# Kernel optimization log

Measured on AMD Instinct MI355X. Metric: run time of the kernel, lower is better.

Reference implementation:

```python
import jax, jax.numpy as jnp
import numpy as np

L, S, R, NUM_RESNET = 6, 2, 3, 3
N = 2 ** L            # 64 blocks per axis
NX = N * S            # 128 grid points per axis
NCART_SIDE = 80
NCART = NCART_SIDE ** 2


def _perm_idx(L_, l):
    delta = 2 ** (L_ - l - 1)
    t = np.tile(np.arange(2) * delta, delta) + np.repeat(np.arange(delta), 2)
    t = np.tile(t, 2 ** l) + np.repeat(np.arange(2 ** l) * 2 ** (L_ - l), 2 ** (L_ - l))
    return jnp.asarray(t)


def _switch_idx(L_):
    h = L_ // 2
    t = np.tile(np.arange(2 ** h) * 2 ** h, 2 ** h) + np.repeat(np.arange(2 ** h), 2 ** h)
    return jnp.asarray(t)


def _bmm2(x, g_left, g_right):
    # x: (B,p,i,q,j). Right block-diag GEMM on (q,j), then left block-diag GEMM on (p,i).
    y = jnp.einsum('bpiqj,qjk->bpiqk', x, g_right)
    return jnp.einsum('bpiqk,pio->bpoqk', y, g_left)


def _complex_layer(xr, xi, p):
    # p: stacked (r1,i1,r2,i2,r3,i3,r4,i4); complex-style cross products of the original.
    r1, i1, r2, i2, r3, i3, r4, i4 = p
    yr = _bmm2(xr, r1, r1) + _bmm2(xr, i1, i1) + _bmm2(xi, r2, i2) + _bmm2(xi, i2, r2)
    yi = _bmm2(xi, r3, r3) + _bmm2(xi, i3, i3) + _bmm2(xr, r4, i4) + _bmm2(xr, i4, r4)
    return yr, yi


def _u_layer(xr, xi, p):
    ur1, ui1, ur2, ui2, ur3, ui3, ur4, ui4 = p
    return (_bmm2(xr, ur1, ur1) + _bmm2(xr, ui2, ui2)
            + _bmm2(xi, ur3, ui3) + _bmm2(xi, ui4, ur4))


def _permute(yr, yi, idx):
    yr = jnp.take(jnp.take(yr, idx, axis=1), idx, axis=3)
    yi = jnp.take(jnp.take(yi, idx, axis=1), idx, axis=3)
    return yr, yi


def _merge(y):  # (B,N,R,N,R) -> (B,N/2,2R,N/2,2R)
    return y.reshape(y.shape[0], N // 2, 2 * R, N // 2, 2 * R)


def _split(y):  # inverse of _merge
    return y.reshape(y.shape[0], N, R, N, R)


def reference(x, Vp, Hp, Mp, Gp, Up, cart_mat, r_index):
    B = x.shape[0]
    xr = x[..., 0].reshape(B, N, S, N, S)
    xi = x[..., 1].reshape(B, N, S, N, S)
    yr, yi = _complex_layer(xr, xi, Vp)                       # (B,N,R,N,R)
    for li, l in enumerate(range(L - 1, L // 2 - 1, -1)):     # H stages (permute then merge-GEMM)
        yr, yi = _permute(yr, yi, _perm_idx(L, l))
        yr, yi = _complex_layer(_merge(yr), _merge(yi), Hp[li])
        yr, yi = _split(yr), _split(yi)
    yr, yi = _permute(yr, yi, _switch_idx(L))                 # middle switch shuffle
    for k in range(NUM_RESNET):                               # residual M blocks
        zr, zi = _complex_layer(yr, yi, Mp[k])
        yr, yi = yr + zr, yi + zi
    for li, l in enumerate(range(L // 2 - 1, -1, -1)):        # G stages (merge-GEMM then permute)
        yr, yi = _complex_layer(_merge(yr), _merge(yi), Gp[li])
        yr, yi = _split(yr), _split(yi)
        yr, yi = _permute(yr, yi, _perm_idx(L, l))
    y = _u_layer(yr, yi, Up).reshape(B, NX * NX)              # real output, (B,NX,NX) flattened
    y = jnp.take(y, r_index, axis=1)                          # polar reindexing
    out = y @ cart_mat.T                                      # polar -> cartesian interpolation
    return out.reshape(B, NCART_SIDE, NCART_SIDE)


def setup_inputs() -> dict:
    key = jax.random.key(0)
    ks = jax.random.split(key, 9)
    B = 128
    x = jax.random.normal(ks[0], (B, NX, NX, 2), dtype=jnp.float32)
    Vp = jax.random.normal(ks[1], (8, N, S, R), dtype=jnp.float32) * 0.35
    Hp = jax.random.normal(ks[2], (L // 2, 8, N // 2, 2 * R, 2 * R), dtype=jnp.float32) * 0.2
    Mp = jax.random.normal(ks[3], (NUM_RESNET, 8, N, R, R), dtype=jnp.float32) * 0.25
    Gp = jax.random.normal(ks[4], (L // 2, 8, N // 2, 2 * R, 2 * R), dtype=jnp.float32) * 0.2
    Up = jax.random.normal(ks[5], (8, N, R, S), dtype=jnp.float32) * 0.35
    cart_mat = jax.random.normal(ks[6], (NCART, NX * NX), dtype=jnp.float32) * 0.01
    r_index = jax.random.permutation(ks[7], NX * NX).astype(jnp.int32)
    return {"x": x, "Vp": Vp, "Hp": Hp, "Mp": Mp, "Gp": Gp, "Up": Up,
            "cart_mat": cart_mat, "r_index": r_index}
```

## Files before the change

kernel.cpp:

```cpp
#include <hip/hip_runtime.h>


typedef _Float16 f16;
typedef __attribute__((ext_vector_type(8))) short sx8;
typedef __attribute__((ext_vector_type(4))) float fx4;
typedef __attribute__((ext_vector_type(8))) unsigned short usx8;
typedef __attribute__((ext_vector_type(4))) unsigned short usx4;

__device__ __forceinline__ unsigned short f2bf(float f) {
  unsigned u = __builtin_bit_cast(unsigned, f);
  u = (u + 0x7FFFu + ((u >> 16) & 1u)) >> 16;
  return (unsigned short)u;
}
__device__ __forceinline__ float bf2f(unsigned short h) {
  return __builtin_bit_cast(float, ((unsigned)h) << 16);
}

template<int ID>
__device__ __forceinline__ int rp_apply(int k) {
  if constexpr (ID == 0) { return k; }
  else if constexpr (ID == 3) { return (k & 7) * 8 + (k >> 3); }
  else {
    constexpr int l = (ID == 1) ? 4 : (ID == 2) ? 3 : (ID == 4) ? 2 : (ID == 5) ? 1 : 0;
    constexpr int d = 1 << (5 - l);
    constexpr int m2 = 2 * d;
    int g = k / m2, r = k % m2;
    return g * m2 + (r & 1) * d + (r >> 1);
  }
}

__device__ __forceinline__ void term_decode(int t, int& lm, int& rm,
                                            bool& useXi, bool& toYi) {
  lm = (t < 2) ? t : (t < 4) ? (t + 4) : (t - 2);
  rm = (t >= 2 && t <= 5) ? (lm ^ 1) : lm;
  useXi = (t >= 4);
  toYi = (t >> 1) & 1;
}

#define SMEM_BYTES 36864

__device__ __forceinline__ void layer6(int g, int b, int P, int Q,
                                       const float* __restrict__ wp,
                                       const f16* ldsX, float* Y0, float* Y1,
                                       f16* __restrict__ yr,
                                       f16* __restrict__ yi) {
  int lm0, rm0, lm1, rm1;
  switch (g) {
    case 0:  lm0 = 0; rm0 = 0; lm1 = 1; rm1 = 1; break;
    case 1:  lm0 = 6; rm0 = 7; lm1 = 7; rm1 = 6; break;
    case 2:  lm0 = 2; rm0 = 3; lm1 = 3; rm1 = 2; break;
    default: lm0 = 4; rm0 = 4; lm1 = 5; rm1 = 5; break;
  }
  const int xbase = (g & 2) ? 36 : 0;
  float X[36], Y[36];
#pragma unroll
  for (int k = 0; k < 36; ++k) X[k] = (float)ldsX[(xbase + k) * 128 + b];
#pragma unroll
  for (int k = 0; k < 36; ++k) Y[k] = 0.f;

  for (int tt = 0; tt < 2; ++tt) {
    const int lm = tt ? lm1 : lm0;
    const int rm = tt ? rm1 : rm0;
    const float* Lw = wp + ((size_t)lm * 32 + P) * 36;
    const float* Rw = wp + ((size_t)rm * 32 + Q) * 36;
#pragma unroll
    for (int i = 0; i < 6; ++i) {
      float tk[6] = {0.f, 0.f, 0.f, 0.f, 0.f, 0.f};
#pragma unroll
      for (int j = 0; j < 6; ++j) {
        float xv = X[i * 6 + j];
#pragma unroll
        for (int k = 0; k < 6; ++k) tk[k] += xv * Rw[j * 6 + k];
      }
#pragma unroll
      for (int o = 0; o < 6; ++o) {
        float lv = Lw[i * 6 + o];
#pragma unroll
        for (int k = 0; k < 6; ++k) Y[o * 6 + k] += lv * tk[k];
      }
    }
  }
  __syncthreads();
  if (g == 2) {
#pragma unroll
    for (int k = 0; k < 36; ++k) Y0[k * 128 + b] = Y[k];
  } else if (g == 3) {
#pragma unroll
    for (int k = 0; k < 36; ++k) Y1[k * 128 + b] = Y[k];
  }
  __syncthreads();
  if (g == 0) {
#pragma unroll
    for (int k = 0; k < 36; ++k) {
      float v = Y[k] + Y0[k * 128 + b];
      yr[((size_t)((P * 6 + k / 6) * 192 + Q * 6 + k % 6)) * 128 + b] = (f16)v;
    }
  } else if (g == 1) {
#pragma unroll
    for (int k = 0; k < 36; ++k) {
      float v = Y[k] + Y1[k * 128 + b];
      yi[((size_t)((P * 6 + k / 6) * 192 + Q * 6 + k % 6)) * 128 + b] = (f16)v;
    }
  }
}

__global__ __launch_bounds__(256) void k_transpose(const float* __restrict__ x,
                                                   f16* __restrict__ xtr,
                                                   f16* __restrict__ xti) {
  __shared__ float ls[2][32][129];
  const int t = threadIdx.x;
  const int u = blockIdx.x;
  const int v0 = blockIdx.y * 32;
  for (int it = 0; it < 32; ++it) {
    int b = it * 4 + (t >> 6);
    int r = t & 63;
    int v = r >> 1, ch = r & 1;
    ls[ch][v][b] = x[(((size_t)b * 128 + u) * 128 + (v0 + v)) * 2 + ch];
  }
  __syncthreads();
  for (int it = 0; it < 32; ++it) {
    int idx = it * 256 + t;
    int ch = idx >> 12;
    int v = (idx >> 7) & 31;
    int b = idx & 127;
    f16* dst = ch ? xti : xtr;
    dst[((size_t)(u * 128 + v0 + v)) * 128 + b] = (f16)ls[ch][v][b];
  }
}

__global__ __launch_bounds__(512, 4) void k_vh(const f16* __restrict__ xtr,
                                               const f16* __restrict__ xti,
                                               f16* __restrict__ yr,
                                               f16* __restrict__ yi,
                                               const float* __restrict__ vp,
                                               const float* __restrict__ hp) {
  __shared__ __align__(16) char smem[SMEM_BYTES];
  f16* ldsX = (f16*)smem;
  float* Y0 = (float*)smem;
  float* Y1 = (float*)(smem + 18432);
  const int t = threadIdx.x;
  const int P = blockIdx.x, Q = blockIdx.y;
  const int g = __builtin_amdgcn_readfirstlane(t >> 7);
  const int b = t & 127;

  const int pp = g >> 1, qq = g & 1;
  const int p = 2 * P + pp, q = 2 * Q + qq;
  float Xr[4], Xi[4];
#pragma unroll
  for (int i = 0; i < 2; ++i)
#pragma unroll
    for (int j = 0; j < 2; ++j) {
      size_t off = ((size_t)((4 * P + 2 * pp + i) * 128 + (4 * Q + 2 * qq + j))) * 128 + b;
      Xr[i * 2 + j] = (float)xtr[off];
      Xi[i * 2 + j] = (float)xti[off];
    }
  float Ar[9], Ai[9];
#pragma unroll
  for (int k = 0; k < 9; ++k) { Ar[k] = 0.f; Ai[k] = 0.f; }
  for (int tt = 0; tt < 8; ++tt) {
    int lm, rm; bool useXi, toYi;
    term_decode(tt, lm, rm, useXi, toYi);
    const float* Lw = vp + ((size_t)lm * 64 + p) * 6;
    const float* Rw = vp + ((size_t)rm * 64 + q) * 6;
#pragma unroll
    for (int i = 0; i < 2; ++i) {
      float x0, x1;
      if (useXi) { x0 = Xi[i * 2 + 0]; x1 = Xi[i * 2 + 1]; }
      else       { x0 = Xr[i * 2 + 0]; x1 = Xr[i * 2 + 1]; }
      float t0 = x0 * Rw[0] + x1 * Rw[3];
      float t1 = x0 * Rw[1] + x1 * Rw[4];
      float t2 = x0 * Rw[2] + x1 * Rw[5];
      if (toYi) {
#pragma unroll
        for (int o = 0; o < 3; ++o) {
          float lv = Lw[i * 3 + o];
          Ai[o*3+0] += lv * t0; Ai[o*3+1] += lv * t1; Ai[o*3+2] += lv * t2;
        }
      } else {
#pragma unroll
        for (int o = 0; o < 3; ++o) {
          float lv = Lw[i * 3 + o];
          Ar[o*3+0] += lv * t0; Ar[o*3+1] += lv * t1; Ar[o*3+2] += lv * t2;
        }
      }
    }
  }
#pragma unroll
  for (int o = 0; o < 3; ++o)
#pragma unroll
    for (int k = 0; k < 3; ++k) {
      int ch = (3 * pp + o) * 6 + (3 * qq + k);
      ldsX[ch * 128 + b] = (f16)Ar[o * 3 + k];
      ldsX[(36 + ch) * 128 + b] = (f16)Ai[o * 3 + k];
    }
  __syncthreads();
  layer6(g, b, P, Q, hp, ldsX, Y0, Y1, yr, yi);
}

template<int PERM>
__global__ __launch_bounds__(512, 4) void k_hg(const f16* __restrict__ xr,
                                               const f16* __restrict__ xi,
                                               f16* __restrict__ yr,
                                               f16* __restrict__ yi,
                                               const float* __restrict__ wp) {
  __shared__ __align__(16) char smem[SMEM_BYTES];
  f16* ldsX = (f16*)smem;
  float* Y0 = (float*)smem;
  float* Y1 = (float*)(smem + 18432);
  const int t = threadIdx.x;
  const int P = blockIdx.x, Q = blockIdx.y;

  for (int r = 0; r < 3; ++r) {
    int idx = t + r * 512;
    if (idx < 1152) {
      int c = idx >> 4, o8 = (idx & 15) * 8;
      int cc = (c < 36) ? c : c - 36;
      int I = cc / 6, J = cc % 6;
      int grow = rp_apply<PERM>(2 * P + I / 3) * 3 + I % 3;
      int gcol = rp_apply<PERM>(2 * Q + J / 3) * 3 + J % 3;
      const f16* src = (c < 36) ? xr : xi;
      usx8 v = *(const usx8*)(src + ((size_t)(grow * 192 + gcol)) * 128 + o8);
      *(usx8*)(ldsX + c * 128 + o8) = v;
    }
  }
  __syncthreads();
  const int g = __builtin_amdgcn_readfirstlane(t >> 7);
  const int b = t & 127;
  layer6(g, b, P, Q, wp, ldsX, Y0, Y1, yr, yi);
}

__global__ __launch_bounds__(512, 4) void k_mg(const f16* __restrict__ xr,
                                               const f16* __restrict__ xi,
                                               f16* __restrict__ yr,
                                               f16* __restrict__ yi,
                                               const float* __restrict__ mp,
                                               const float* __restrict__ gp) {
  __shared__ __align__(16) char smem[SMEM_BYTES];
  f16* ldsX = (f16*)smem;
  float* Y0 = (float*)smem;
  float* Y1 = (float*)(smem + 18432);
  const int t = threadIdx.x;
  const int P = blockIdx.x, Q = blockIdx.y;
  const int g = __builtin_amdgcn_readfirstlane(t >> 7);
  const int b = t & 127;

  const int aa = g >> 1, bb = g & 1;
  const int p = 2 * P + aa, q = 2 * Q + bb;
  const int prow = rp_apply<3>(p) * 3, pcol = rp_apply<3>(q) * 3;
  float Xr[9], Xi[9];
#pragma unroll
  for (int i = 0; i < 3; ++i)
#pragma unroll
    for (int j = 0; j < 3; ++j) {
      size_t off = ((size_t)((prow + i) * 192 + (pcol + j))) * 128 + b;
      Xr[i * 3 + j] = (float)xr[off];
      Xi[i * 3 + j] = (float)xi[off];
    }
  for (int lk = 0; lk < 3; ++lk) {
    const float* wp = mp + (size_t)lk * (8 * 64 * 9);
    float Yr9[9], Yi9[9];
#pragma unroll
    for (int k = 0; k < 9; ++k) { Yr9[k] = Xr[k]; Yi9[k] = Xi[k]; }
    for (int tt = 0; tt < 8; ++tt) {
      int lm, rm; bool useXi, toYi;
      term_decode(tt, lm, rm, useXi, toYi);
      const float* Lw = wp + ((size_t)lm * 64 + p) * 9;
      const float* Rw = wp + ((size_t)rm * 64 + q) * 9;
#pragma unroll
      for (int i = 0; i < 3; ++i) {
        float x0, x1, x2;
        if (useXi) { x0 = Xi[i*3+0]; x1 = Xi[i*3+1]; x2 = Xi[i*3+2]; }
        else       { x0 = Xr[i*3+0]; x1 = Xr[i*3+1]; x2 = Xr[i*3+2]; }
        float t0 = x0 * Rw[0] + x1 * Rw[3] + x2 * Rw[6];
        float t1 = x0 * Rw[1] + x1 * Rw[4] + x2 * Rw[7];
        float t2 = x0 * Rw[2] + x1 * Rw[5] + x2 * Rw[8];
        if (toYi) {
#pragma unroll
          for (int o = 0; o < 3; ++o) {
            float lv = Lw[i * 3 + o];
            Yi9[o*3+0] += lv * t0; Yi9[o*3+1] += lv * t1; Yi9[o*3+2] += lv * t2;
          }
        } else {
#pragma unroll
          for (int o = 0; o < 3; ++o) {
            float lv = Lw[i * 3 + o];
            Yr9[o*3+0] += lv * t0; Yr9[o*3+1] += lv * t1; Yr9[o*3+2] += lv * t2;
          }
        }
      }
    }
#pragma unroll
    for (int k = 0; k < 9; ++k) { Xr[k] = Yr9[k]; Xi[k] = Yi9[k]; }
  }
#pragma unroll
  for (int i = 0; i < 3; ++i)
#pragma unroll
    for (int j = 0; j < 3; ++j) {
      int ch = (3 * aa + i) * 6 + (3 * bb + j);
      ldsX[ch * 128 + b] = (f16)Xr[i * 3 + j];
      ldsX[(36 + ch) * 128 + b] = (f16)Xi[i * 3 + j];
    }
  __syncthreads();
  layer6(g, b, P, Q, gp, ldsX, Y0, Y1, yr, yi);
}

__global__ __launch_bounds__(128, 2) void k_u(const f16* __restrict__ xr,
                                              const f16* __restrict__ xi,
                                              unsigned short* __restrict__ ut,
                                              const float* __restrict__ wp) {
  const int b = threadIdx.x;
  const int p = blockIdx.x, q = blockIdx.y;
  int rrow[3], rcol[3];
#pragma unroll
  for (int i = 0; i < 3; ++i) {
    rrow[i] = rp_apply<6>(p) * 3 + i;
    rcol[i] = rp_apply<6>(q) * 3 + i;
  }
  float X[9], Y[4] = {0.f, 0.f, 0.f, 0.f};
  auto loadX = [&](const f16* src) {
#pragma unroll
    for (int i = 0; i < 3; ++i)
#pragma unroll
      for (int j = 0; j < 3; ++j)
        X[i * 3 + j] = (float)src[((size_t)(rrow[i] * 192 + rcol[j])) * 128 + b];
  };
  auto term = [&](int lm, int rm) {
    const float* Lw = wp + ((size_t)lm * 64 + p) * 6;
    const float* Rw = wp + ((size_t)rm * 64 + q) * 6;
#pragma unroll
    for (int i = 0; i < 3; ++i) {
      float t0 = X[i*3+0] * Rw[0] + X[i*3+1] * Rw[2] + X[i*3+2] * Rw[4];
      float t1 = X[i*3+0] * Rw[1] + X[i*3+1] * Rw[3] + X[i*3+2] * Rw[5];
      Y[0] += Lw[i*2+0] * t0; Y[1] += Lw[i*2+0] * t1;
      Y[2] += Lw[i*2+1] * t0; Y[3] += Lw[i*2+1] * t1;
    }
  };
  loadX(xr); term(0, 0); term(3, 3);
  loadX(xi); term(4, 5); term(7, 6);
#pragma unroll
  for (int o = 0; o < 2; ++o)
#pragma unroll
    for (int k = 0; k < 2; ++k)
      ut[((size_t)((p * 2 + o) * 128 + (q * 2 + k))) * 128 + b] = f2bf(Y[o * 2 + k]);
}

__global__ __launch_bounds__(256) void k_gather(const unsigned short* __restrict__ ut,
                                                const int* __restrict__ r_index,
                                                unsigned short* __restrict__ yg) {
  __shared__ unsigned short ls[64][130];
  __shared__ int ridx[64];
  const int t = threadIdx.x;
  const int m0 = blockIdx.x * 64;
  if (t < 64) ridx[t] = r_index[m0 + t];
  __syncthreads();
  for (int it = 0; it < 32; ++it) {
    int idx = it * 256 + t;
    int ml = idx >> 7, b = idx & 127;
    ls[ml][b] = ut[(size_t)ridx[ml] * 128 + b];
  }
  __syncthreads();
  int b = t >> 1, half = t & 1;
#pragma unroll
  for (int c = 0; c < 4; ++c) {
    usx8 v;
#pragma unroll
    for (int e = 0; e < 8; ++e) v[e] = ls[half * 32 + c * 8 + e][b];
    *(usx8*)(yg + (size_t)b * 16384 + m0 + half * 32 + c * 8) = v;
  }
}

#define G3_KC 8
#define G3_STEPS 32
#define G3_PITCH 72

__global__ __launch_bounds__(256) void k_gemm3(const unsigned short* __restrict__ yg,
                                               const float* __restrict__ cart,
                                               unsigned short* __restrict__ partial) {
  __shared__ unsigned short Bs[2][64][G3_PITCH];
  const int t = threadIdx.x;
  const int lane = t & 63, w = t >> 6;
  const int kc = blockIdx.x;
  const int c0 = blockIdx.y * 64;
  const int k0 = kc * 2048;

  fx4 acc[2][4];
#pragma unroll
  for (int i = 0; i < 2; ++i)
#pragma unroll
    for (int j = 0; j < 4; ++j) acc[i][j] = (fx4)0.f;

  const unsigned short* aBase = yg + (size_t)(w * 32 + (lane & 15)) * 16384
                                   + k0 + (lane >> 4) * 8;

  auto ldB = [&](int rep, int kpos, fx4* f0, fx4* f1) {
    int c = t + rep * 256;
    const float* p = cart + (size_t)(c0 + (c >> 3)) * 16384 + kpos + (c & 7) * 8;
    *f0 = *(const fx4*)p;
    *f1 = *(const fx4*)(p + 4);
  };
  auto stB = [&](int buf, int rep, fx4 f0, fx4 f1) {
    int c = t + rep * 256;
    usx8 v;
    v[0]=f2bf(f0[0]); v[1]=f2bf(f0[1]); v[2]=f2bf(f0[2]); v[3]=f2bf(f0[3]);
    v[4]=f2bf(f1[0]); v[5]=f2bf(f1[1]); v[6]=f2bf(f1[2]); v[7]=f2bf(f1[3]);
    *(usx8*)(&Bs[buf][c >> 3][(c & 7) * 8]) = v;
  };

  {
    fx4 b00, b01, b10, b11;
    ldB(0, k0, &b00, &b01); ldB(1, k0, &b10, &b11);
    stB(0, 0, b00, b01); stB(0, 1, b10, b11);
  }
  __syncthreads();

  for (int s = 0; s < G3_STEPS; ++s) {
    const int cur = s & 1;
    fx4 b00, b01, b10, b11;
    const bool pf = (s + 1 < G3_STEPS);
    if (pf) {
      int kpos = k0 + (s + 1) * 64;
      ldB(0, kpos, &b00, &b01); ldB(1, kpos, &b10, &b11);
    }
    sx8 af[2][2], bf[4][2];
#pragma unroll
    for (int mi = 0; mi < 2; ++mi)
#pragma unroll
      for (int kk = 0; kk < 2; ++kk)
        af[mi][kk] = *(const sx8*)(aBase + (size_t)mi * 16 * 16384 + s * 64 + kk * 32);
#pragma unroll
    for (int ni = 0; ni < 4; ++ni)
#pragma unroll
      for (int kk = 0; kk < 2; ++kk)
        bf[ni][kk] = *(const sx8*)(&Bs[cur][ni * 16 + (lane & 15)][kk * 32 + (lane >> 4) * 8]);
#pragma unroll
    for (int kk = 0; kk < 2; ++kk)
#pragma unroll
      for (int mi = 0; mi < 2; ++mi)
#pragma unroll
        for (int ni = 0; ni < 4; ++ni)
          acc[mi][ni] = __builtin_amdgcn_mfma_f32_16x16x32_bf16(af[mi][kk], bf[ni][kk], acc[mi][ni], 0, 0, 0);
    if (pf) {
      stB(cur ^ 1, 0, b00, b01); stB(cur ^ 1, 1, b10, b11);
    }
    __syncthreads();
  }

#pragma unroll
  for (int mi = 0; mi < 2; ++mi) {
    int brow = w * 32 + mi * 16 + (lane >> 4) * 4;
#pragma unroll
    for (int ni = 0; ni < 4; ++ni) {
      int cc = c0 + ni * 16 + (lane & 15);
#pragma unroll
      for (int r = 0; r < 4; ++r)
        partial[((size_t)kc * 128 + brow + r) * 6400 + cc] = f2bf(acc[mi][ni][r]);
    }
  }
}

__global__ __launch_bounds__(256) void k_reduce2(const unsigned short* __restrict__ partial,
                                                 float* __restrict__ out) {
  int i = blockIdx.x * 256 + threadIdx.x;
  fx4 s = (fx4)0.f;
#pragma unroll
  for (int kc = 0; kc < G3_KC; ++kc) {
    usx4 v = *(const usx4*)(partial + (size_t)kc * 819200 + (size_t)i * 4);
    s[0] += bf2f(v[0]); s[1] += bf2f(v[1]); s[2] += bf2f(v[2]); s[3] += bf2f(v[3]);
  }
  *(fx4*)(out + (size_t)i * 4) = s;
}

extern "C" void kernel_launch(void* const* d_in, const int* in_sizes, int n_in,
                              void* d_out, int out_size, void* d_ws, size_t ws_size,
                              hipStream_t stream) {
  const float* x    = (const float*)d_in[0];
  const float* Vp   = (const float*)d_in[1];
  const float* Hp   = (const float*)d_in[2];
  const float* Mp   = (const float*)d_in[3];
  const float* Gp   = (const float*)d_in[4];
  const float* Up   = (const float*)d_in[5];
  const float* cart = (const float*)d_in[6];
  const int*   ridx = (const int*)d_in[7];
  float* out = (float*)d_out;
  unsigned short* hb = (unsigned short*)d_ws;

  const size_t PSZ = 4718592;
  f16* P0r = (f16*)(hb);
  f16* P0i = (f16*)(hb + PSZ);
  f16* P1r = (f16*)(hb + 2 * PSZ);
  f16* P1i = (f16*)(hb + 3 * PSZ);
  f16* xtr = (f16*)(hb + 4 * PSZ);
  f16* xti = (f16*)(hb + 4 * PSZ + 2097152);
  unsigned short* ut = hb + 4 * PSZ;
  unsigned short* yg = hb + 4 * PSZ + 2097152;
  unsigned short* partial = hb;

  const size_t HSZ = 8 * 32 * 36;

  k_transpose<<<dim3(128, 4), 256, 0, stream>>>(x, xtr, xti);
  k_vh<<<dim3(32, 32), 512, 0, stream>>>(xtr, xti, P0r, P0i, Vp, Hp + 0 * HSZ);
  k_hg<1><<<dim3(32, 32), 512, 0, stream>>>(P0r, P0i, P1r, P1i, Hp + 1 * HSZ);
  k_hg<2><<<dim3(32, 32), 512, 0, stream>>>(P1r, P1i, P0r, P0i, Hp + 2 * HSZ);
  k_mg<<<dim3(32, 32), 512, 0, stream>>>(P0r, P0i, P1r, P1i, Mp, Gp + 0 * HSZ);
  k_hg<4><<<dim3(32, 32), 512, 0, stream>>>(P1r, P1i, P0r, P0i, Gp + 1 * HSZ);
  k_hg<5><<<dim3(32, 32), 512, 0, stream>>>(P0r, P0i, P1r, P1i, Gp + 2 * HSZ);
  k_u<<<dim3(64, 64), 128, 0, stream>>>(P1r, P1i, ut, Up);
  k_gather<<<dim3(256), 256, 0, stream>>>(ut, ridx, yg);
  k_gemm3<<<dim3(G3_KC, 100), 256, 0, stream>>>(yg, cart, partial);
  k_reduce2<<<dim3(800), 256, 0, stream>>>(partial, out);
  (void)in_sizes; (void)n_in; (void)out_size; (void)ws_size;
}
```

Measured before the change: 308.6 us.

## Stage A tiles through LDS and deepen cartesian GEMM prefetch pipeline

The final polar-to-cartesian GEMM now loads A (the gathered activations) into shared memory cooperatively instead of having each wave read fragments straight from global memory. It also halves the K step to 32 and adds a register-staged, two-step-ahead prefetch, with a triple-buffered B and a double-buffered A. The goal is to hide global-load latency and make A reads coalesced. In exchange it does twice as many iterations and barriers, uses more shared memory, and keeps more registers live for the prefetch.

```diff
diff --git a/kernel.cpp b/kernel.cpp
--- a/kernel.cpp
+++ b/kernel.cpp
@@ -369,14 +369,15 @@
   }
 }
 
-#define G3_KC 8
-#define G3_STEPS 32
-#define G3_PITCH 72
-
-__global__ __launch_bounds__(256) void k_gemm3(const unsigned short* __restrict__ yg,
+#define G4_KC 8
+#define G4_STEPS 64
+#define G4_P 40
+
+__global__ __launch_bounds__(256) void k_gemm4(const unsigned short* __restrict__ yg,
                                                const float* __restrict__ cart,
                                                unsigned short* __restrict__ partial) {
-  __shared__ unsigned short Bs[2][64][G3_PITCH];
+  __shared__ unsigned short As[2][128][G4_P];
+  __shared__ unsigned short Bs[3][64][G4_P];
   const int t = threadIdx.x;
   const int lane = t & 63, w = t >> 6;
   const int kc = blockIdx.x;
@@ -389,59 +390,56 @@
 #pragma unroll
     for (int j = 0; j < 4; ++j) acc[i][j] = (fx4)0.f;
 
-  const unsigned short* aBase = yg + (size_t)(w * 32 + (lane & 15)) * 16384
-                                   + k0 + (lane >> 4) * 8;
-
-  auto ldB = [&](int rep, int kpos, fx4* f0, fx4* f1) {
-    int c = t + rep * 256;
-    const float* p = cart + (size_t)(c0 + (c >> 3)) * 16384 + kpos + (c & 7) * 8;
+  auto ldA = [&](int kpos, usx8* a0, usx8* a1) {
+    int c0i = t, c1i = t + 256;
+    *a0 = *(const usx8*)(yg + (size_t)(c0i >> 2) * 16384 + kpos + (c0i & 3) * 8);
+    *a1 = *(const usx8*)(yg + (size_t)(c1i >> 2) * 16384 + kpos + (c1i & 3) * 8);
+  };
+  auto stA = [&](int buf, usx8 a0, usx8 a1) {
+    int c0i = t, c1i = t + 256;
+    *(usx8*)(&As[buf][c0i >> 2][(c0i & 3) * 8]) = a0;
+    *(usx8*)(&As[buf][c1i >> 2][(c1i & 3) * 8]) = a1;
+  };
+  auto ldB = [&](int kpos, fx4* f0, fx4* f1) {
+    const float* p = cart + (size_t)(c0 + (t >> 2)) * 16384 + kpos + (t & 3) * 8;
     *f0 = *(const fx4*)p;
     *f1 = *(const fx4*)(p + 4);
   };
-  auto stB = [&](int buf, int rep, fx4 f0, fx4 f1) {
-    int c = t + rep * 256;
+  auto stB = [&](int buf, fx4 f0, fx4 f1) {
     usx8 v;
     v[0]=f2bf(f0[0]); v[1]=f2bf(f0[1]); v[2]=f2bf(f0[2]); v[3]=f2bf(f0[3]);
     v[4]=f2bf(f1[0]); v[5]=f2bf(f1[1]); v[6]=f2bf(f1[2]); v[7]=f2bf(f1[3]);
-    *(usx8*)(&Bs[buf][c >> 3][(c & 7) * 8]) = v;
+    *(usx8*)(&Bs[buf][t >> 2][(t & 3) * 8]) = v;
   };
 
+  usx8 rA0, rA1; fx4 rB0, rB1;
   {
-    fx4 b00, b01, b10, b11;
-    ldB(0, k0, &b00, &b01); ldB(1, k0, &b10, &b11);
-    stB(0, 0, b00, b01); stB(0, 1, b10, b11);
-  }
-  __syncthreads();
-
-  for (int s = 0; s < G3_STEPS; ++s) {
-    const int cur = s & 1;
-    fx4 b00, b01, b10, b11;
-    const bool pf = (s + 1 < G3_STEPS);
-    if (pf) {
-      int kpos = k0 + (s + 1) * 64;
-      ldB(0, kpos, &b00, &b01); ldB(1, kpos, &b10, &b11);
-    }
-    sx8 af[2][2], bf[4][2];
+    usx8 pa0, pa1; fx4 pb0, pb1;
+    ldA(k0, &pa0, &pa1); ldB(k0, &pb0, &pb1);
+    ldA(k0 + 32, &rA0, &rA1); ldB(k0 + 32, &rB0, &rB1);
+    stA(0, pa0, pa1); stB(0, pb0, pb1);
+  }
+  __syncthreads();
+
+  for (int s = 0; s < G4_STEPS; ++s) {
+    const int curA = s & 1, curB = s % 3;
+    if (s + 1 < G4_STEPS) { stB((s + 1) % 3, rB0, rB1); stA((s + 1) & 1, rA0, rA1); }
+    if (s + 2 < G4_STEPS) {
+      ldB(k0 + (s + 2) * 32, &rB0, &rB1);
+      ldA(k0 + (s + 2) * 32, &rA0, &rA1);
+    }
+    sx8 af[2], bf[4];
 #pragma unroll
     for (int mi = 0; mi < 2; ++mi)
-#pragma unroll
-      for (int kk = 0; kk < 2; ++kk)
-        af[mi][kk] = *(const sx8*)(aBase + (size_t)mi * 16 * 16384 + s * 64 + kk * 32);
+      af[mi] = *(const sx8*)(&As[curA][w * 32 + mi * 16 + (lane & 15)][(lane >> 4) * 8]);
 #pragma unroll
     for (int ni = 0; ni < 4; ++ni)
-#pragma unroll
-      for (int kk = 0; kk < 2; ++kk)
-        bf[ni][kk] = *(const sx8*)(&Bs[cur][ni * 16 + (lane & 15)][kk * 32 + (lane >> 4) * 8]);
-#pragma unroll
-    for (int kk = 0; kk < 2; ++kk)
-#pragma unroll
-      for (int mi = 0; mi < 2; ++mi)
-#pragma unroll
-        for (int ni = 0; ni < 4; ++ni)
-          acc[mi][ni] = __builtin_amdgcn_mfma_f32_16x16x32_bf16(af[mi][kk], bf[ni][kk], acc[mi][ni], 0, 0, 0);
-    if (pf) {
-      stB(cur ^ 1, 0, b00, b01); stB(cur ^ 1, 1, b10, b11);
-    }
+      bf[ni] = *(const sx8*)(&Bs[curB][ni * 16 + (lane & 15)][(lane >> 4) * 8]);
+#pragma unroll
+    for (int mi = 0; mi < 2; ++mi)
+#pragma unroll
+      for (int ni = 0; ni < 4; ++ni)
+        acc[mi][ni] = __builtin_amdgcn_mfma_f32_16x16x32_bf16(af[mi], bf[ni], acc[mi][ni], 0, 0, 0);
     __syncthreads();
   }
 
@@ -463,7 +461,7 @@
   int i = blockIdx.x * 256 + threadIdx.x;
   fx4 s = (fx4)0.f;
 #pragma unroll
-  for (int kc = 0; kc < G3_KC; ++kc) {
+  for (int kc = 0; kc < G4_KC; ++kc) {
     usx4 v = *(const usx4*)(partial + (size_t)kc * 819200 + (size_t)i * 4);
     s[0] += bf2f(v[0]); s[1] += bf2f(v[1]); s[2] += bf2f(v[2]); s[3] += bf2f(v[3]);
   }
@@ -506,7 +504,7 @@
   k_hg<5><<<dim3(32, 32), 512, 0, stream>>>(P0r, P0i, P1r, P1i, Gp + 2 * HSZ);
   k_u<<<dim3(64, 64), 128, 0, stream>>>(P1r, P1i, ut, Up);
   k_gather<<<dim3(256), 256, 0, stream>>>(ut, ridx, yg);
-  k_gemm3<<<dim3(G3_KC, 100), 256, 0, stream>>>(yg, cart, partial);
+  k_gemm4<<<dim3(G4_KC, 100), 256, 0, stream>>>(yg, cart, partial);
   k_reduce2<<<dim3(800), 256, 0, stream>>>(partial, out);
   (void)in_sizes; (void)n_in; (void)out_size; (void)ws_size;
 }
```

Measured after the change: 322.9 us. 1.05x slower.
